# Kernel optimization log

Measured on AMD Instinct MI355X. Metric: run time of the kernel, lower is better.

## Reference

```python
import jax, jax.numpy as jnp
import numpy as np

N_NODES = 100000
N_EDGES = 1600000
NUM_FEAT = 128
HIDDEN = 64
NUM_OUT = 21


def gcn_conv(x, src, dst, norm, W, b, n):
    # PyG GCNConv: h = x @ W (no bias in lin); aggregate normalized messages; add bias.
    h = x @ W  # [N, out]
    msg = h[src] * norm[:, None]  # gather + scale, [E+N, out]
    out = jax.ops.segment_sum(msg, dst, num_segments=n)  # scatter-add, [N, out]
    return out + b


def gcn_norm(edge_index, n, dtype):
    # Add self-loops, compute symmetric normalization deg^-1/2[src]*deg^-1/2[dst].
    loop = jnp.arange(n, dtype=edge_index.dtype)
    src = jnp.concatenate([edge_index[0], loop])
    dst = jnp.concatenate([edge_index[1], loop])
    deg = jax.ops.segment_sum(jnp.ones_like(dst, dtype=dtype), dst, num_segments=n)
    dinv = jnp.where(deg > 0, deg ** -0.5, 0.0).astype(dtype)
    norm = dinv[src] * dinv[dst]
    return src, dst, norm


def setup_inputs() -> dict:
    key = jax.random.key(0)
    k1, k2, k3, k4, k5 = jax.random.split(key, 5)
    x = jax.random.normal(k1, (N_NODES, NUM_FEAT), dtype=jnp.float32)
    edge_index = jax.random.randint(k2, (2, N_EDGES), 0, N_NODES, dtype=jnp.int64)
    s1 = 1.0 / np.sqrt(NUM_FEAT)
    s2 = 1.0 / np.sqrt(HIDDEN)
    W1 = jax.random.uniform(k3, (NUM_FEAT, HIDDEN), jnp.float32, -s1, s1)
    b1 = jnp.zeros((HIDDEN,), jnp.float32)
    W2 = jax.random.uniform(k4, (HIDDEN, NUM_OUT), jnp.float32, -s2, s2)
    b2 = jnp.zeros((NUM_OUT,), jnp.float32)
    return {"x": x, "edge_index": edge_index, "W1": W1, "b1": b1, "W2": W2, "b2": b2}


def reference(x, edge_index, W1, b1, W2, b2):
    n = x.shape[0]
    src, dst, norm = gcn_norm(edge_index, n, x.dtype)
    h = gcn_conv(x, src, dst, norm, W1, b1, n)
    h = jax.nn.relu(h)
    out = gcn_conv(h, src, dst, norm, W2, b2, n)
    return out
```

## Files before the change

### kernel.cpp

```cpp
#include <hip/hip_runtime.h>

#define NFEAT 128
#define NHID  64
#define NOUT  21
#define BSH   7
#define BCAP  8192
#define CHUNK 4096
#define EPT   (CHUNK/256)
#define PADI  16
#define NBUKMAX 1024

typedef unsigned int uint;
typedef unsigned short ushort_t;

typedef __bf16 bf16_t;
typedef bf16_t bf16x8 __attribute__((ext_vector_type(8)));
typedef float  f32x4  __attribute__((ext_vector_type(4)));

__device__ inline uint packbf2(float a, float b) {
    uint ua = __float_as_uint(a), ub = __float_as_uint(b);
    ua = (ua + 0x7FFFu + ((ua >> 16) & 1u)) >> 16;
    ub = (ub + 0x7FFFu + ((ub >> 16) & 1u)) >> 16;
    return ua | (ub << 16);
}
__device__ inline float bflo(uint v) { return __uint_as_float(v << 16); }
__device__ inline float bfhi(uint v) { return __uint_as_float(v & 0xffff0000u); }


__global__ __launch_bounds__(256) void k_lsort(const int* __restrict__ src, const int* __restrict__ dst,
                                               uint* __restrict__ ebuf, int* __restrict__ tab,
                                               int* __restrict__ gcnt, int E, int nbuk) {
    __shared__ int  lcnt[NBUKMAX + 1];
    __shared__ int  lsum[256];
    __shared__ uint lsorted[CHUNK];
    int c = blockIdx.x, tid = threadIdx.x;
    int base = c * CHUNK;
    int ccnt = min(CHUNK, E - base);

    for (int j = tid; j <= nbuk; j += 256) lcnt[j] = 0;
    __syncthreads();

    int  buk[EPT];
    uint rec[EPT];
#pragma unroll
    for (int k = 0; k < EPT; ++k) {
        int e = base + k * 256 + tid;
        if (e < E) {
            int d = dst[e];
            buk[k] = d >> BSH;
            rec[k] = ((uint)(d & ((1 << BSH) - 1)) << 17) | (uint)src[e];
            atomicAdd(&lcnt[buk[k]], 1);
        }
    }
    __syncthreads();

    int g = (nbuk + 255) / 256;
    int j0 = tid * g;
    int s = 0;
    for (int j = 0; j < g; ++j) { int idx = j0 + j; if (idx < nbuk) s += lcnt[idx]; }
    lsum[tid] = s;
    __syncthreads();
    for (int off = 1; off < 256; off <<= 1) {
        int t = (tid >= off) ? lsum[tid - off] : 0;
        __syncthreads();
        lsum[tid] += t;
        __syncthreads();
    }
    int run = lsum[tid] - s;
    for (int j = 0; j < g; ++j) {
        int idx = j0 + j;
        if (idx < nbuk) { int cv = lcnt[idx]; lcnt[idx] = run; run += cv; }
    }
    __syncthreads();
    if (tid == 0) lcnt[nbuk] = ccnt;
    __syncthreads();

    for (int j = tid; j < nbuk; j += 256) {
        int st = lcnt[j];
        tab[(size_t)c * (nbuk + 1) + j] = st;
        int cj = lcnt[j + 1] - st;
        if (cj) atomicAdd(&gcnt[j * PADI], cj);
    }
    if (tid == 0) tab[(size_t)c * (nbuk + 1) + nbuk] = ccnt;
    __syncthreads();

#pragma unroll
    for (int k = 0; k < EPT; ++k) {
        int e = base + k * 256 + tid;
        if (e < E) {
            int pos = atomicAdd(&lcnt[buk[k]], 1);
            lsorted[pos] = rec[k];
        }
    }
    __syncthreads();
    for (int i = tid; i < ccnt; i += 256) ebuf[base + i] = lsorted[i];
}


__global__ __launch_bounds__(256) void k_bscan(const int* __restrict__ gcnt, int* __restrict__ bbase,
                                               int* __restrict__ rowptr, int nbuk, int N, int E) {
    __shared__ int lv[NBUKMAX];
    __shared__ int lsum[256];
    int tid = threadIdx.x;
    int g = (nbuk + 255) / 256;
    int j0 = tid * g;
    int s = 0;
    for (int j = 0; j < g; ++j) {
        int idx = j0 + j;
        int v = (idx < nbuk) ? gcnt[idx * PADI] : 0;
        if (idx < nbuk) lv[idx] = v;
        s += v;
    }
    lsum[tid] = s;
    __syncthreads();
    for (int off = 1; off < 256; off <<= 1) {
        int t = (tid >= off) ? lsum[tid - off] : 0;
        __syncthreads();
        lsum[tid] += t;
        __syncthreads();
    }
    int run = lsum[tid] - s;
    for (int j = 0; j < g; ++j) {
        int idx = j0 + j;
        if (idx < nbuk) { bbase[idx] = run; run += lv[idx]; }
    }
    if (tid == 0) rowptr[N] = E;
}


__global__ __launch_bounds__(256) void k_bsort2(const uint* __restrict__ ebuf, const int* __restrict__ tab,
                                                const int* __restrict__ bbase_, const int* __restrict__ gcnt,
                                                int* __restrict__ rowptr, float* __restrict__ dinv,
                                                int* __restrict__ esrc, int nchunk, int nbuk, int N) {
    __shared__ int  ncnt[128];
    __shared__ int  sc[128];
    __shared__ int  lcur[128];
    __shared__ uint stash[BCAP];
    __shared__ int  lpos;
    int b = blockIdx.x, tid = threadIdx.x;
    int nb0 = b << BSH;
    int bb = bbase_[b];
    int cnt_b = gcnt[b * PADI];
    bool fits = (cnt_b <= BCAP);

    if (tid < 128) ncnt[tid] = 0;
    if (tid == 0) lpos = 0;
    __syncthreads();

    for (int c = tid; c < nchunk; c += 256) {
        const int* trow = tab + (size_t)c * (nbuk + 1);
        int s0 = trow[b], e0 = trow[b + 1];
        int len = e0 - s0;
        if (len <= 0) continue;
        const uint* pb = ebuf + (size_t)c * CHUNK;
        if (fits) {
            int pos = atomicAdd(&lpos, len);
            for (int i = 0; i < len; ++i) {
                uint r = pb[s0 + i];
                stash[pos + i] = r;
                atomicAdd(&ncnt[r >> 17], 1);
            }
        } else {
            for (int i = 0; i < len; ++i) atomicAdd(&ncnt[pb[s0 + i] >> 17], 1);
        }
    }
    __syncthreads();

    int v = (tid < 128) ? ncnt[tid] : 0;
    if (tid < 128) sc[tid] = v;
    __syncthreads();
    for (int off = 1; off < 128; off <<= 1) {
        int t = (tid >= off && tid < 128) ? sc[tid - off] : 0;
        __syncthreads();
        if (tid < 128) sc[tid] += t;
        __syncthreads();
    }
    if (tid < 128) {
        int excl = sc[tid] - v;
        int node = nb0 + tid;
        if (node < N) {
            rowptr[node] = bb + excl;
            dinv[node] = rsqrtf((float)(v + 1));
        }
        lcur[tid] = bb + excl;
    }
    __syncthreads();

    if (fits) {
        for (int i = tid; i < cnt_b; i += 256) {
            uint r = stash[i];
            int pos = atomicAdd(&lcur[r >> 17], 1);
            esrc[pos] = (int)(r & 0x1FFFFu);
        }
    } else {
        for (int c = tid; c < nchunk; c += 256) {
            const int* trow = tab + (size_t)c * (nbuk + 1);
            int s0 = trow[b], e0 = trow[b + 1];
            const uint* pb = ebuf + (size_t)c * CHUNK;
            for (int i = s0; i < e0; ++i) {
                uint r = pb[i];
                int pos = atomicAdd(&lcur[r >> 17], 1);
                esrc[pos] = (int)(r & 0x1FFFFu);
            }
        }
    }
}


__global__ __launch_bounds__(256) void k_count(const int* __restrict__ dst, int* cnt, int E) {
    int e = blockIdx.x * 256 + threadIdx.x;
    if (e < E) atomicAdd(&cnt[dst[e]], 1);
}

__global__ __launch_bounds__(256) void k_scan1(const int* __restrict__ cnt, int* __restrict__ rowptr,
                                               int* __restrict__ bsum, float* __restrict__ dinv, int N) {
    __shared__ int sh[256];
    int tid = threadIdx.x;
    int base = blockIdx.x * 1024 + tid * 4;
    int v[4]; int s = 0;
#pragma unroll
    for (int j = 0; j < 4; ++j) {
        v[j] = (base + j < N) ? cnt[base + j] : 0;
        if (base + j < N) dinv[base + j] = rsqrtf((float)(v[j] + 1));
        s += v[j];
    }
    sh[tid] = s; __syncthreads();
    for (int off = 1; off < 256; off <<= 1) {
        int t = (tid >= off) ? sh[tid - off] : 0;
        __syncthreads();
        sh[tid] += t;
        __syncthreads();
    }
    int run = sh[tid] - s;
#pragma unroll
    for (int j = 0; j < 4; ++j) { if (base + j < N) rowptr[base + j] = run; run += v[j]; }
    if (tid == 255) bsum[blockIdx.x] = sh[255];
}

__global__ __launch_bounds__(128) void k_scan2(int* bsum, int nb) {
    __shared__ int sh[128];
    int tid = threadIdx.x;
    int v = (tid < nb) ? bsum[tid] : 0;
    sh[tid] = v; __syncthreads();
    for (int off = 1; off < 128; off <<= 1) {
        int t = (tid >= off) ? sh[tid - off] : 0;
        __syncthreads();
        sh[tid] += t;
        __syncthreads();
    }
    if (tid < nb) bsum[tid] = sh[tid] - v;
}

__global__ __launch_bounds__(256) void k_scan3(int* __restrict__ rowptr, int* __restrict__ fill,
                                               const int* __restrict__ bsum, int N, int E) {
    int tid = threadIdx.x;
    int base = blockIdx.x * 1024 + tid * 4;
    int add = bsum[blockIdx.x];
#pragma unroll
    for (int j = 0; j < 4; ++j) {
        int idx = base + j;
        if (idx < N) {
            int r = rowptr[idx] + add;
            rowptr[idx] = r;
            fill[idx] = r;
        }
    }
    if (blockIdx.x == 0 && tid == 0) rowptr[N] = E;
}

__global__ __launch_bounds__(256) void k_scatter_direct(const int* __restrict__ src, const int* __restrict__ dst,
                                                        int* __restrict__ fill, int* __restrict__ esrc, int E) {
    int e = blockIdx.x * 256 + threadIdx.x;
    if (e >= E) return;
    int pos = atomicAdd(&fill[dst[e]], 1);
    esrc[pos] = src[e];
}


__global__ __launch_bounds__(256) void k_gemm1(const float* __restrict__ x, const float* __restrict__ W1,
                                               const float* __restrict__ dinv, uint* __restrict__ hb, int N) {
    __shared__ ushort_t xs[64 * 136];
    __shared__ ushort_t ws[64 * 136];
    int tid = threadIdx.x;
    int r0 = blockIdx.x * 64;

    {
        int col = tid & 63;
        int kb = (tid >> 6) * 32;
#pragma unroll
        for (int kk = 0; kk < 32; kk += 2) {
            float a = W1[(size_t)(kb + kk) * NHID + col];
            float b = W1[(size_t)(kb + kk + 1) * NHID + col];
            *(uint*)&ws[col * 136 + kb + kk] = packbf2(a, b);
        }
    }
    {
        int row = tid >> 2;
        int q = tid & 3;
        int grow = r0 + row;
        uint buf[16];
        if (grow < N) {
            const float* xr = x + (size_t)grow * NFEAT + q * 32;
#pragma unroll
            for (int j = 0; j < 8; ++j) {
                float4 v = *(const float4*)&xr[j * 4];
                buf[2 * j]     = packbf2(v.x, v.y);
                buf[2 * j + 1] = packbf2(v.z, v.w);
            }
        } else {
#pragma unroll
            for (int j = 0; j < 16; ++j) buf[j] = 0u;
        }
        uint* d = (uint*)&xs[row * 136 + q * 32];
#pragma unroll
        for (int j = 0; j < 4; ++j)
            ((uint4*)d)[j] = make_uint4(buf[4 * j], buf[4 * j + 1], buf[4 * j + 2], buf[4 * j + 3]);
    }
    __syncthreads();

    int lane = tid & 63;
    int wrow = (tid >> 6) * 16;
    int lrow = lane & 15;
    int lk   = (lane >> 4) * 8;

    f32x4 acc[4];
#pragma unroll
    for (int nt = 0; nt < 4; ++nt) acc[nt] = (f32x4){0.f, 0.f, 0.f, 0.f};

#pragma unroll
    for (int kq = 0; kq < 4; ++kq) {
        int k0 = kq * 32;
        bf16x8 a = *(const bf16x8*)&xs[(wrow + lrow) * 136 + k0 + lk];
#pragma unroll
        for (int nt = 0; nt < 4; ++nt) {
            bf16x8 b = *(const bf16x8*)&ws[(nt * 16 + lrow) * 136 + k0 + lk];
            acc[nt] = __builtin_amdgcn_mfma_f32_16x16x32_bf16(a, b, acc[nt], 0, 0, 0);
        }
    }

    int orow0 = (lane >> 4) * 4;
    float dvv[4];
#pragma unroll
    for (int r = 0; r < 4; ++r) {
        int grow = r0 + wrow + orow0 + r;
        dvv[r] = (grow < N) ? dinv[grow] : 0.f;
    }
    ushort_t* hbs = (ushort_t*)hb;
#pragma unroll
    for (int nt = 0; nt < 4; ++nt) {
#pragma unroll
        for (int r = 0; r < 4; ++r) {
            int grow = r0 + wrow + orow0 + r;
            if (grow < N) {
                uint pb = packbf2(acc[nt][r] * dvv[r], 0.f);
                hbs[(size_t)grow * 64 + nt * 16 + lrow] = (ushort_t)(pb & 0xffffu);
            }
        }
    }
}


__global__ __launch_bounds__(256) void k_agg1(const int* __restrict__ rowptr, const int* __restrict__ esrc,
                                              const uint* __restrict__ hb, const float* __restrict__ dinv,
                                              const float* __restrict__ b1, uint* __restrict__ o1b, int N) {
    int tid = threadIdx.x;
    int node = blockIdx.x * 4 + (tid >> 6);
    if (node >= N) return;
    int lane = tid & 63;
    int half = lane >> 5;
    int c = lane & 31;
    uint sv = hb[(size_t)node * 32 + c];
    float ax = half ? 0.f : bflo(sv);
    float ay = half ? 0.f : bfhi(sv);
    int beg = rowptr[node], end = rowptr[node + 1];
    int i = beg + half;
    for (; i + 14 < end; i += 16) {
        int s0 = esrc[i], s1 = esrc[i + 2], s2 = esrc[i + 4], s3 = esrc[i + 6];
        int s4 = esrc[i + 8], s5 = esrc[i + 10], s6 = esrc[i + 12], s7 = esrc[i + 14];
        uint v0 = hb[(size_t)s0 * 32 + c];
        uint v1 = hb[(size_t)s1 * 32 + c];
        uint v2 = hb[(size_t)s2 * 32 + c];
        uint v3 = hb[(size_t)s3 * 32 + c];
        uint v4 = hb[(size_t)s4 * 32 + c];
        uint v5 = hb[(size_t)s5 * 32 + c];
        uint v6 = hb[(size_t)s6 * 32 + c];
        uint v7 = hb[(size_t)s7 * 32 + c];
        ax += bflo(v0) + bflo(v1);
        ay += bfhi(v0) + bfhi(v1);
        ax += bflo(v2) + bflo(v3);
        ay += bfhi(v2) + bfhi(v3);
        ax += bflo(v4) + bflo(v5);
        ay += bfhi(v4) + bfhi(v5);
        ax += bflo(v6) + bflo(v7);
        ay += bfhi(v6) + bfhi(v7);
    }
    for (; i + 6 < end; i += 8) {
        int s0 = esrc[i], s1 = esrc[i + 2], s2 = esrc[i + 4], s3 = esrc[i + 6];
        uint v0 = hb[(size_t)s0 * 32 + c];
        uint v1 = hb[(size_t)s1 * 32 + c];
        uint v2 = hb[(size_t)s2 * 32 + c];
        uint v3 = hb[(size_t)s3 * 32 + c];
        ax += bflo(v0) + bflo(v1);
        ay += bfhi(v0) + bfhi(v1);
        ax += bflo(v2) + bflo(v3);
        ay += bfhi(v2) + bfhi(v3);
    }
    for (; i < end; i += 2) {
        uint v = hb[(size_t)esrc[i] * 32 + c];
        ax += bflo(v); ay += bfhi(v);
    }
    ax += __shfl_xor(ax, 32);
    ay += __shfl_xor(ay, 32);
    if (!half) {
        float dv = dinv[node];
        float2 bv = ((const float2*)b1)[c];
        float rx = fmaxf(fmaf(ax, dv, bv.x), 0.f);
        float ry = fmaxf(fmaf(ay, dv, bv.y), 0.f);
        o1b[(size_t)node * 32 + c] = packbf2(rx, ry);
    }
}


__global__ __launch_bounds__(256) void k_gemm2m(const uint* __restrict__ o1b, const float* __restrict__ W2,
                                                const float* __restrict__ dinv, uint* __restrict__ h2b, int N) {
    __shared__ ushort_t xs[64 * 136];
    __shared__ ushort_t ws[32 * 136];
    int tid = threadIdx.x;
    int r0 = blockIdx.x * 64;

    {
        int col = tid & 31;
        int kb = (tid >> 5) * 8;
#pragma unroll
        for (int kk = 0; kk < 8; kk += 2) {
            float a = (col < NOUT) ? W2[(size_t)(kb + kk) * NOUT + col] : 0.f;
            float b = (col < NOUT) ? W2[(size_t)(kb + kk + 1) * NOUT + col] : 0.f;
            *(uint*)&ws[col * 136 + kb + kk] = packbf2(a, b);
        }
    }
    {
        int row = tid >> 2;
        int q = tid & 3;
        int grow = r0 + row;
        uint4 v0 = make_uint4(0u, 0u, 0u, 0u), v1 = v0;
        if (grow < N) {
            const uint4* sp = (const uint4*)(o1b + (size_t)grow * 32 + q * 8);
            v0 = sp[0]; v1 = sp[1];
        }
        uint* d = (uint*)&xs[row * 136 + q * 16];
        ((uint4*)d)[0] = v0;
        ((uint4*)d)[1] = v1;
    }
    __syncthreads();

    int lane = tid & 63;
    int wrow = (tid >> 6) * 16;
    int lrow = lane & 15;
    int lk   = (lane >> 4) * 8;

    f32x4 acc[2];
#pragma unroll
    for (int nt = 0; nt < 2; ++nt) acc[nt] = (f32x4){0.f, 0.f, 0.f, 0.f};

#pragma unroll
    for (int kq = 0; kq < 2; ++kq) {
        int k0 = kq * 32;
        bf16x8 a = *(const bf16x8*)&xs[(wrow + lrow) * 136 + k0 + lk];
#pragma unroll
        for (int nt = 0; nt < 2; ++nt) {
            bf16x8 b = *(const bf16x8*)&ws[(nt * 16 + lrow) * 136 + k0 + lk];
            acc[nt] = __builtin_amdgcn_mfma_f32_16x16x32_bf16(a, b, acc[nt], 0, 0, 0);
        }
    }

    int orow0 = (lane >> 4) * 4;
    float dvv[4];
#pragma unroll
    for (int r = 0; r < 4; ++r) {
        int grow = r0 + wrow + orow0 + r;
        dvv[r] = (grow < N) ? dinv[grow] : 0.f;
    }
    ushort_t* h2s = (ushort_t*)h2b;
#pragma unroll
    for (int nt = 0; nt < 2; ++nt) {
#pragma unroll
        for (int r = 0; r < 4; ++r) {
            int grow = r0 + wrow + orow0 + r;
            if (grow < N) {
                uint pb = packbf2(acc[nt][r] * dvv[r], 0.f);
                h2s[(size_t)grow * 32 + nt * 16 + lrow] = (ushort_t)(pb & 0xffffu);
            }
        }
    }
}


__global__ __launch_bounds__(256) void k_agg2(const int* __restrict__ rowptr, const int* __restrict__ esrc,
                                              const uint* __restrict__ h2b, const float* __restrict__ dinv,
                                              const float* __restrict__ b2, float* __restrict__ out, int N) {
    int tid = threadIdx.x;
    int node = blockIdx.x * 64 + (tid >> 2);
    if (node >= N) return;
    int q = tid & 3;
    uint4 sv = *((const uint4*)(h2b + (size_t)node * 16) + q);
    float a0 = bflo(sv.x), a1 = bfhi(sv.x), a2 = bflo(sv.y), a3 = bfhi(sv.y);
    float a4 = bflo(sv.z), a5 = bfhi(sv.z), a6 = bflo(sv.w), a7 = bfhi(sv.w);
    int beg = rowptr[node], end = rowptr[node + 1];
    int i = beg;
    for (; i + 3 < end; i += 4) {
        int s0 = esrc[i], s1 = esrc[i + 1], s2 = esrc[i + 2], s3 = esrc[i + 3];
        uint4 v0 = *((const uint4*)(h2b + (size_t)s0 * 16) + q);
        uint4 v1 = *((const uint4*)(h2b + (size_t)s1 * 16) + q);
        uint4 v2 = *((const uint4*)(h2b + (size_t)s2 * 16) + q);
        uint4 v3 = *((const uint4*)(h2b + (size_t)s3 * 16) + q);
        a0 += bflo(v0.x) + bflo(v1.x);
        a1 += bfhi(v0.x) + bfhi(v1.x);
        a2 += bflo(v0.y) + bflo(v1.y);
        a3 += bfhi(v0.y) + bfhi(v1.y);
        a4 += bflo(v0.z) + bflo(v1.z);
        a5 += bfhi(v0.z) + bfhi(v1.z);
        a6 += bflo(v0.w) + bflo(v1.w);
        a7 += bfhi(v0.w) + bfhi(v1.w);
        a0 += bflo(v2.x) + bflo(v3.x);
        a1 += bfhi(v2.x) + bfhi(v3.x);
        a2 += bflo(v2.y) + bflo(v3.y);
        a3 += bfhi(v2.y) + bfhi(v3.y);
        a4 += bflo(v2.z) + bflo(v3.z);
        a5 += bfhi(v2.z) + bfhi(v3.z);
        a6 += bflo(v2.w) + bflo(v3.w);
        a7 += bfhi(v2.w) + bfhi(v3.w);
    }
    for (; i < end; ++i) {
        uint4 v0 = *((const uint4*)(h2b + (size_t)esrc[i] * 16) + q);
        a0 += bflo(v0.x); a1 += bfhi(v0.x);
        a2 += bflo(v0.y); a3 += bfhi(v0.y);
        a4 += bflo(v0.z); a5 += bfhi(v0.z);
        a6 += bflo(v0.w); a7 += bfhi(v0.w);
    }
    float dv = dinv[node];
    float* orow = out + (size_t)node * NOUT;
    int col = q * 8;
    float av[8] = {a0, a1, a2, a3, a4, a5, a6, a7};
#pragma unroll
    for (int j = 0; j < 8; ++j)
        if (col + j < NOUT) orow[col + j] = fmaf(dv, av[j], b2[col + j]);
}


extern "C" void kernel_launch(void* const* d_in, const int* in_sizes, int n_in,
                              void* d_out, int out_size, void* d_ws, size_t ws_size,
                              hipStream_t stream) {
    const float* x  = (const float*)d_in[0];
    const int*   ei = (const int*)d_in[1];
    const float* W1 = (const float*)d_in[2];
    const float* b1 = (const float*)d_in[3];
    const float* W2 = (const float*)d_in[4];
    const float* b2 = (const float*)d_in[5];
    float* out = (float*)d_out;

    int N = in_sizes[0] / NFEAT;
    int E = in_sizes[1] / 2;
    const int* src = ei;
    const int* dst = ei + E;
    int NBUK = (N + (1 << BSH) - 1) >> BSH;
    int NCHUNK = (E + CHUNK - 1) / CHUNK;

    char* p = (char*)d_ws;
    auto alloc = [&](size_t bytes) { void* r = (void*)p; p += (bytes + 255) & ~(size_t)255; return r; };
    int*   rowptr = (int*)alloc((size_t)(N + 1) * 4);
    int*   gcnt   = (int*)alloc((size_t)NBUK * PADI * 4);
    int*   bbase  = (int*)alloc((size_t)NBUK * 4);
    int*   tab    = (int*)alloc((size_t)NCHUNK * (NBUK + 1) * 4);
    uint*  ebuf   = (uint*)alloc((size_t)E * 4);
    int*   esrc   = (int*)alloc((size_t)E * 4);
    float* dinv   = (float*)alloc((size_t)N * 4);
    uint*  hb     = (uint*)alloc((size_t)N * 32 * 4);
    uint*  o1b    = (uint*)alloc((size_t)N * 32 * 4);
    uint*  h2b    = (uint*)alloc((size_t)N * 16 * 4);
    int*   cnt    = (int*)alloc((size_t)N * 4);
    int*   fill   = (int*)alloc((size_t)N * 4);
    int*   bsum   = (int*)alloc(128 * 4);

    const int B = 256;

    if (N <= (1 << 17)) {
        hipMemsetAsync(gcnt, 0, (size_t)NBUK * PADI * 4, stream);
        k_lsort <<<NCHUNK, 256, 0, stream>>>(src, dst, ebuf, tab, gcnt, E, NBUK);
        k_bscan <<<1, 256, 0, stream>>>(gcnt, bbase, rowptr, NBUK, N, E);
        k_bsort2<<<NBUK, 256, 0, stream>>>(ebuf, tab, bbase, gcnt, rowptr, dinv, esrc, NCHUNK, NBUK, N);
    } else {
        int nb = (N + 1023) / 1024;
        hipMemsetAsync(cnt, 0, (size_t)N * 4, stream);
        k_count <<<(E + B - 1) / B, B, 0, stream>>>(dst, cnt, E);
        k_scan1 <<<nb, 256, 0, stream>>>(cnt, rowptr, bsum, dinv, N);
        k_scan2 <<<1, 128, 0, stream>>>(bsum, nb);
        k_scan3 <<<nb, 256, 0, stream>>>(rowptr, fill, bsum, N, E);
        k_scatter_direct<<<(E + B - 1) / B, B, 0, stream>>>(src, dst, fill, esrc, E);
    }

    k_gemm1 <<<(N + 63) / 64, 256, 0, stream>>>(x, W1, dinv, hb, N);
    k_agg1  <<<(N + 3) / 4, 256, 0, stream>>>(rowptr, esrc, hb, dinv, b1, o1b, N);
    k_gemm2m<<<(N + 63) / 64, 256, 0, stream>>>(o1b, W2, dinv, h2b, N);
    k_agg2  <<<(N + 63) / 64, 256, 0, stream>>>(rowptr, esrc, h2b, dinv, b2, out, N);
}
```

Before: 164.5 us.

## Vectorize local sort I/O, fold bucket scan into bsort2, enlarge gemm1 tile

Vectorizes the edge loads and the sorted-chunk writeback in k_lsort with int4/uint4 accesses. It also removes the single-block k_bscan launch: each k_bsort2 block computes its own bucket base by reducing the preceding gcnt entries. k_gemm1 now processes 128 rows per block, with two MFMA row tiles per wave that reuse the same W fragments. This saves a launch and some memory transactions, but each block redoes a prefix sum over up to ~780 buckets and gemm1 uses more LDS and registers.

```diff
diff --git a/kernel.cpp b/kernel.cpp
--- a/kernel.cpp
+++ b/kernel.cpp
@@ -6,7 +6,7 @@
 #define BSH   7
 #define BCAP  8192
 #define CHUNK 4096
-#define EPT   (CHUNK/256)
+#define EPT   16
 #define PADI  16
 #define NBUKMAX 1024
 
@@ -43,13 +43,29 @@
     int  buk[EPT];
     uint rec[EPT];
 #pragma unroll
-    for (int k = 0; k < EPT; ++k) {
-        int e = base + k * 256 + tid;
-        if (e < E) {
-            int d = dst[e];
-            buk[k] = d >> BSH;
-            rec[k] = ((uint)(d & ((1 << BSH) - 1)) << 17) | (uint)src[e];
-            atomicAdd(&lcnt[buk[k]], 1);
+    for (int g = 0; g < EPT / 4; ++g) {
+        int e0 = base + g * 1024 + tid * 4;
+        int4 dv, sv;
+        if (e0 + 3 < E) {
+            dv = *(const int4*)&dst[e0];
+            sv = *(const int4*)&src[e0];
+        } else {
+            dv = make_int4(0, 0, 0, 0); sv = dv;
+            if (e0     < E) { dv.x = dst[e0];     sv.x = src[e0]; }
+            if (e0 + 1 < E) { dv.y = dst[e0 + 1]; sv.y = src[e0 + 1]; }
+            if (e0 + 2 < E) { dv.z = dst[e0 + 2]; sv.z = src[e0 + 2]; }
+        }
+        int dd[4] = {dv.x, dv.y, dv.z, dv.w};
+        int ss[4] = {sv.x, sv.y, sv.z, sv.w};
+#pragma unroll
+        for (int j = 0; j < 4; ++j) {
+            int k = g * 4 + j;
+            buk[k] = -1;
+            if (e0 + j < E) {
+                buk[k] = dd[j] >> BSH;
+                rec[k] = ((uint)(dd[j] & ((1 << BSH) - 1)) << 17) | (uint)ss[j];
+                atomicAdd(&lcnt[buk[k]], 1);
+            }
         }
     }
     __syncthreads();
@@ -86,65 +102,49 @@
 
 #pragma unroll
     for (int k = 0; k < EPT; ++k) {
-        int e = base + k * 256 + tid;
-        if (e < E) {
+        if (buk[k] >= 0) {
             int pos = atomicAdd(&lcnt[buk[k]], 1);
             lsorted[pos] = rec[k];
         }
     }
     __syncthreads();
-    for (int i = tid; i < ccnt; i += 256) ebuf[base + i] = lsorted[i];
-}
-
-
-__global__ __launch_bounds__(256) void k_bscan(const int* __restrict__ gcnt, int* __restrict__ bbase,
-                                               int* __restrict__ rowptr, int nbuk, int N, int E) {
-    __shared__ int lv[NBUKMAX];
-    __shared__ int lsum[256];
-    int tid = threadIdx.x;
-    int g = (nbuk + 255) / 256;
-    int j0 = tid * g;
-    int s = 0;
-    for (int j = 0; j < g; ++j) {
-        int idx = j0 + j;
-        int v = (idx < nbuk) ? gcnt[idx * PADI] : 0;
-        if (idx < nbuk) lv[idx] = v;
-        s += v;
-    }
-    lsum[tid] = s;
-    __syncthreads();
-    for (int off = 1; off < 256; off <<= 1) {
-        int t = (tid >= off) ? lsum[tid - off] : 0;
-        __syncthreads();
-        lsum[tid] += t;
-        __syncthreads();
-    }
-    int run = lsum[tid] - s;
-    for (int j = 0; j < g; ++j) {
-        int idx = j0 + j;
-        if (idx < nbuk) { bbase[idx] = run; run += lv[idx]; }
-    }
-    if (tid == 0) rowptr[N] = E;
+    for (int i = tid * 4; i + 3 < ccnt; i += 1024)
+        *(uint4*)&ebuf[base + i] = *(uint4*)&lsorted[i];
+    int tail = ccnt & ~3;
+    for (int i = tail + tid; i < ccnt; i += 256) ebuf[base + i] = lsorted[i];
 }
 
 
 __global__ __launch_bounds__(256) void k_bsort2(const uint* __restrict__ ebuf, const int* __restrict__ tab,
-                                                const int* __restrict__ bbase_, const int* __restrict__ gcnt,
+                                                const int* __restrict__ gcnt,
                                                 int* __restrict__ rowptr, float* __restrict__ dinv,
-                                                int* __restrict__ esrc, int nchunk, int nbuk, int N) {
+                                                int* __restrict__ esrc, int nchunk, int nbuk, int N, int E) {
     __shared__ int  ncnt[128];
     __shared__ int  sc[128];
     __shared__ int  lcur[128];
+    __shared__ int  rsum[256];
     __shared__ uint stash[BCAP];
     __shared__ int  lpos;
     int b = blockIdx.x, tid = threadIdx.x;
     int nb0 = b << BSH;
-    int bb = bbase_[b];
     int cnt_b = gcnt[b * PADI];
     bool fits = (cnt_b <= BCAP);
 
+    int ps = 0;
+    for (int j = tid; j < b; j += 256) ps += gcnt[j * PADI];
+    rsum[tid] = ps;
+    __syncthreads();
+    for (int off = 128; off >= 1; off >>= 1) {
+        if (tid < off) rsum[tid] += rsum[tid + off];
+        __syncthreads();
+    }
+    int bb = rsum[0];
+
     if (tid < 128) ncnt[tid] = 0;
-    if (tid == 0) lpos = 0;
+    if (tid == 0) {
+        lpos = 0;
+        if (b == nbuk - 1) rowptr[N] = E;
+    }
     __syncthreads();
 
     for (int c = tid; c < nchunk; c += 256) {
@@ -279,10 +279,10 @@
 
 __global__ __launch_bounds__(256) void k_gemm1(const float* __restrict__ x, const float* __restrict__ W1,
                                                const float* __restrict__ dinv, uint* __restrict__ hb, int N) {
-    __shared__ ushort_t xs[64 * 136];
+    __shared__ ushort_t xs[128 * 136];
     __shared__ ushort_t ws[64 * 136];
     int tid = threadIdx.x;
-    int r0 = blockIdx.x * 64;
+    int r0 = blockIdx.x * 128;
 
     {
         int col = tid & 63;
@@ -295,65 +295,72 @@
         }
     }
     {
-        int row = tid >> 2;
-        int q = tid & 3;
+        int row = tid >> 1;
+        int h = tid & 1;
         int grow = r0 + row;
-        uint buf[16];
+        uint buf[32];
         if (grow < N) {
-            const float* xr = x + (size_t)grow * NFEAT + q * 32;
-#pragma unroll
-            for (int j = 0; j < 8; ++j) {
+            const float* xr = x + (size_t)grow * NFEAT + h * 64;
+#pragma unroll
+            for (int j = 0; j < 16; ++j) {
                 float4 v = *(const float4*)&xr[j * 4];
                 buf[2 * j]     = packbf2(v.x, v.y);
                 buf[2 * j + 1] = packbf2(v.z, v.w);
             }
         } else {
 #pragma unroll
-            for (int j = 0; j < 16; ++j) buf[j] = 0u;
-        }
-        uint* d = (uint*)&xs[row * 136 + q * 32];
-#pragma unroll
-        for (int j = 0; j < 4; ++j)
+            for (int j = 0; j < 32; ++j) buf[j] = 0u;
+        }
+        uint* d = (uint*)&xs[row * 136 + h * 64];
+#pragma unroll
+        for (int j = 0; j < 8; ++j)
             ((uint4*)d)[j] = make_uint4(buf[4 * j], buf[4 * j + 1], buf[4 * j + 2], buf[4 * j + 3]);
     }
     __syncthreads();
 
     int lane = tid & 63;
-    int wrow = (tid >> 6) * 16;
+    int w = tid >> 6;
     int lrow = lane & 15;
     int lk   = (lane >> 4) * 8;
 
-    f32x4 acc[4];
-#pragma unroll
-    for (int nt = 0; nt < 4; ++nt) acc[nt] = (f32x4){0.f, 0.f, 0.f, 0.f};
+    f32x4 acc[2][4];
+#pragma unroll
+    for (int s = 0; s < 2; ++s)
+#pragma unroll
+        for (int nt = 0; nt < 4; ++nt) acc[s][nt] = (f32x4){0.f, 0.f, 0.f, 0.f};
 
 #pragma unroll
     for (int kq = 0; kq < 4; ++kq) {
         int k0 = kq * 32;
-        bf16x8 a = *(const bf16x8*)&xs[(wrow + lrow) * 136 + k0 + lk];
+        bf16x8 a0 = *(const bf16x8*)&xs[(w * 32 + lrow) * 136 + k0 + lk];
+        bf16x8 a1 = *(const bf16x8*)&xs[(w * 32 + 16 + lrow) * 136 + k0 + lk];
 #pragma unroll
         for (int nt = 0; nt < 4; ++nt) {
             bf16x8 b = *(const bf16x8*)&ws[(nt * 16 + lrow) * 136 + k0 + lk];
-            acc[nt] = __builtin_amdgcn_mfma_f32_16x16x32_bf16(a, b, acc[nt], 0, 0, 0);
+            acc[0][nt] = __builtin_amdgcn_mfma_f32_16x16x32_bf16(a0, b, acc[0][nt], 0, 0, 0);
+            acc[1][nt] = __builtin_amdgcn_mfma_f32_16x16x32_bf16(a1, b, acc[1][nt], 0, 0, 0);
         }
     }
 
     int orow0 = (lane >> 4) * 4;
-    float dvv[4];
-#pragma unroll
-    for (int r = 0; r < 4; ++r) {
-        int grow = r0 + wrow + orow0 + r;
-        dvv[r] = (grow < N) ? dinv[grow] : 0.f;
-    }
     ushort_t* hbs = (ushort_t*)hb;
 #pragma unroll
-    for (int nt = 0; nt < 4; ++nt) {
+    for (int s = 0; s < 2; ++s) {
+        float dvv[4];
 #pragma unroll
         for (int r = 0; r < 4; ++r) {
-            int grow = r0 + wrow + orow0 + r;
-            if (grow < N) {
-                uint pb = packbf2(acc[nt][r] * dvv[r], 0.f);
-                hbs[(size_t)grow * 64 + nt * 16 + lrow] = (ushort_t)(pb & 0xffffu);
+            int grow = r0 + w * 32 + s * 16 + orow0 + r;
+            dvv[r] = (grow < N) ? dinv[grow] : 0.f;
+        }
+#pragma unroll
+        for (int nt = 0; nt < 4; ++nt) {
+#pragma unroll
+            for (int r = 0; r < 4; ++r) {
+                int grow = r0 + w * 32 + s * 16 + orow0 + r;
+                if (grow < N) {
+                    uint pb = packbf2(acc[s][nt][r] * dvv[r], 0.f);
+                    hbs[(size_t)grow * 64 + nt * 16 + lrow] = (ushort_t)(pb & 0xffffu);
+                }
             }
         }
     }
@@ -569,7 +576,6 @@
     auto alloc = [&](size_t bytes) { void* r = (void*)p; p += (bytes + 255) & ~(size_t)255; return r; };
     int*   rowptr = (int*)alloc((size_t)(N + 1) * 4);
     int*   gcnt   = (int*)alloc((size_t)NBUK * PADI * 4);
-    int*   bbase  = (int*)alloc((size_t)NBUK * 4);
     int*   tab    = (int*)alloc((size_t)NCHUNK * (NBUK + 1) * 4);
     uint*  ebuf   = (uint*)alloc((size_t)E * 4);
     int*   esrc   = (int*)alloc((size_t)E * 4);
@@ -586,8 +592,7 @@
     if (N <= (1 << 17)) {
         hipMemsetAsync(gcnt, 0, (size_t)NBUK * PADI * 4, stream);
         k_lsort <<<NCHUNK, 256, 0, stream>>>(src, dst, ebuf, tab, gcnt, E, NBUK);
-        k_bscan <<<1, 256, 0, stream>>>(gcnt, bbase, rowptr, NBUK, N, E);
-        k_bsort2<<<NBUK, 256, 0, stream>>>(ebuf, tab, bbase, gcnt, rowptr, dinv, esrc, NCHUNK, NBUK, N);
+        k_bsort2<<<NBUK, 256, 0, stream>>>(ebuf, tab, gcnt, rowptr, dinv, esrc, NCHUNK, NBUK, N, E);
     } else {
         int nb = (N + 1023) / 1024;
         hipMemsetAsync(cnt, 0, (size_t)N * 4, stream);
@@ -598,7 +603,7 @@
         k_scatter_direct<<<(E + B - 1) / B, B, 0, stream>>>(src, dst, fill, esrc, E);
     }
 
-    k_gemm1 <<<(N + 63) / 64, 256, 0, stream>>>(x, W1, dinv, hb, N);
+    k_gemm1 <<<(N + 127) / 128, 256, 0, stream>>>(x, W1, dinv, hb, N);
     k_agg1  <<<(N + 3) / 4, 256, 0, stream>>>(rowptr, esrc, hb, dinv, b1, o1b, N);
     k_gemm2m<<<(N + 63) / 64, 256, 0, stream>>>(o1b, W2, dinv, h2b, N);
     k_agg2  <<<(N + 63) / 64, 256, 0, stream>>>(rowptr, esrc, h2b, dinv, b2, out, N);
```

Result: no change. 163.5 us (-0.6%).
